# Kernel optimization log

Hardware: AMD Instinct MI355X
Metric: run time of the kernel (lower is better)

## Reference

```python
import jax, jax.numpy as jnp
import numpy as np

D = 768      # num_hiddens (hardcoded by dense1/dense2/ln in the source)
H = 12       # num_heads
NEG = -1000000.0
EPS = 1e-5


def setup_inputs() -> dict:
    key = jax.random.key(0)
    ks = jax.random.split(key, 14)
    B, Lq, Lk = 8, 1024, 1024
    s = 0.02
    return {
        "queries": jax.random.normal(ks[0], (B, Lq, D), dtype=jnp.float32),
        "keys":    jax.random.normal(ks[1], (B, Lk, D), dtype=jnp.float32),
        "values":  jax.random.normal(ks[2], (B, Lk, D), dtype=jnp.float32),
        # binary padding masks; count_nonzero along axis 1 gives valid lens
        "mask_1": jax.random.randint(ks[3], (B, Lk), 0, 2, dtype=jnp.int32),
        "mask_2": jax.random.randint(ks[4], (B, Lq), 0, 2, dtype=jnp.int32),
        # projection weights stored as [in, out] (torch Linear is y = x @ W.T)
        "Wq": jax.random.normal(ks[5], (D, D), dtype=jnp.float32) * s,
        "Wk": jax.random.normal(ks[6], (D, D), dtype=jnp.float32) * s,
        "Wv": jax.random.normal(ks[7], (D, D), dtype=jnp.float32) * s,
        "Wo": jax.random.normal(ks[8], (D, D), dtype=jnp.float32) * s,
        "d1_w": jax.random.normal(ks[9], (D, D), dtype=jnp.float32) * s,
        "d1_b": jnp.zeros((D,), dtype=jnp.float32),
        "d2_w": jax.random.normal(ks[10], (D, D), dtype=jnp.float32) * s,
        "d2_b": jnp.zeros((D,), dtype=jnp.float32),
        "ln_g": jnp.ones((D,), dtype=jnp.float32),
        "ln_b": jnp.zeros((D,), dtype=jnp.float32),
    }


def _cross_att(queries, keys, values, mask_1, mask_2,
               Wq, Wk, Wv, Wo, d1_w, d1_b, d2_w, d2_b, ln_g, ln_b):
    B, Lq, _ = queries.shape
    Lk = keys.shape[1]
    hd = D // H
    # project + split heads: [B, H, L, hd]
    q = (queries @ Wq).reshape(B, Lq, H, hd).transpose(0, 2, 1, 3)
    k = (keys    @ Wk).reshape(B, Lk, H, hd).transpose(0, 2, 1, 3)
    v = (values  @ Wv).reshape(B, Lk, H, hd).transpose(0, 2, 1, 3)
    scores = jnp.einsum('bhqd,bhkd->bhqk', q, k) / jnp.sqrt(jnp.float32(hd))
    # dual-axis prefix mask from nonzero counts
    vl1 = jnp.sum(mask_1 != 0, axis=1)  # [B], masks key axis
    vl2 = jnp.sum(mask_2 != 0, axis=1)  # [B], masks query axis
    col_ok = jnp.arange(Lk)[None, None, None, :] < vl1[:, None, None, None]
    row_ok = jnp.arange(Lq)[None, None, :, None] < vl2[:, None, None, None]
    scores = jnp.where(col_ok & row_ok, scores, NEG)
    attn = jax.nn.softmax(scores, axis=-1)
    out = jnp.einsum('bhqk,bhkd->bhqd', attn, v)
    out = out.transpose(0, 2, 1, 3).reshape(B, Lq, D)
    mha = out @ Wo
    ffn = jax.nn.relu(mha @ d1_w + d1_b) @ d2_w + d2_b
    x = ffn + mha  # dropout is identity in eval
    mu = jnp.mean(x, axis=-1, keepdims=True)
    var = jnp.mean(jnp.square(x - mu), axis=-1, keepdims=True)
    return (x - mu) / jnp.sqrt(var + EPS) * ln_g + ln_b


def reference(queries, keys, values, mask_1, mask_2,
              Wq, Wk, Wv, Wo, d1_w, d1_b, d2_w, d2_b, ln_g, ln_b):
    return _cross_att(queries, keys, values, mask_1, mask_2,
                      Wq, Wk, Wv, Wo, d1_w, d1_b, d2_w, d2_b, ln_g, ln_b)
```

## Files before the change

### kernel.cpp

```cpp
#include <hip/hip_runtime.h>
#include <hip/hip_bf16.h>
#include <type_traits>

#define DM   768
#define NH   12
#define HD   64
#define BATCH 8
#define SEQ  1024
#define NROWS (BATCH * SEQ)

typedef short bf16x8 __attribute__((ext_vector_type(8)));
typedef float f32x4 __attribute__((ext_vector_type(4)));

__device__ inline unsigned short f2b(float x) {
    union { float f; unsigned int u; } v; v.f = x;
    return (unsigned short)((v.u + 0x8000u) >> 16);
}
__device__ inline unsigned int f2b2(float lo, float hi) {
    union { float f; unsigned int u; } a, b; a.f = lo; b.f = hi;
    return __builtin_amdgcn_perm(b.u + 0x8000u, a.u + 0x8000u, 0x07060302u);
}
__device__ inline float b2f(unsigned short u) {
    union { float f; unsigned int x; } v; v.x = ((unsigned int)u) << 16;
    return v.f;
}

__device__ inline void gld16(const unsigned short* g, unsigned short* l) {
    __builtin_amdgcn_global_load_lds(
        (const __attribute__((address_space(1))) unsigned int*)g,
        (__attribute__((address_space(3))) unsigned int*)l, 16, 0, 0);
}

__global__ __launch_bounds__(256) void prep_kernel(const float* __restrict__ w0,
                                                   const float* __restrict__ w1,
                                                   const float* __restrict__ w2,
                                                   const float* __restrict__ w3,
                                                   const float* __restrict__ w4,
                                                   const float* __restrict__ w5,
                                                   unsigned short* __restrict__ wt,
                                                   const int* __restrict__ m1,
                                                   const int* __restrict__ m2,
                                                   int* __restrict__ lens) {
    const int z = blockIdx.z;
    const int t = threadIdx.x;

    if (z < 6) {
        __shared__ float tile[32][33];
        const float* W = (z == 0) ? w0 : (z == 1) ? w1 : (z == 2) ? w2
                       : (z == 3) ? w3 : (z == 4) ? w4 : w5;
        unsigned short* Wt = wt + (size_t)z * DM * DM;
        const int n0 = blockIdx.x * 32;
        const int k0 = blockIdx.y * 32;
        const int tx = t & 31;
        const int ty = t >> 5;
#pragma unroll
        for (int r = 0; r < 4; ++r)
            tile[ty + 8 * r][tx] = W[(size_t)(k0 + ty + 8 * r) * DM + n0 + tx];
        __syncthreads();
#pragma unroll
        for (int r = 0; r < 4; ++r)
            Wt[(size_t)(n0 + ty + 8 * r) * DM + k0 + tx] = f2b(tile[tx][ty + 8 * r]);
        return;
    }

    if (blockIdx.y == 12) {
        if (blockIdx.x >= 16) return;
        __shared__ int redi[256];
        const int bid = blockIdx.x;
        const int b = bid & 7;
        const int* m = (bid < 8) ? m1 : m2;
        int cnt = 0;
        for (int i = t; i < SEQ; i += 256) cnt += (m[b * SEQ + i] != 0) ? 1 : 0;
        redi[t] = cnt;
        __syncthreads();
        for (int off = 128; off > 0; off >>= 1) {
            if (t < off) redi[t] += redi[t + off];
            __syncthreads();
        }
        if (t == 0) lens[bid] = redi[0];
        return;
    }

    if (blockIdx.x >= 12 || blockIdx.y >= 12) return;
    {
        __shared__ __align__(16) unsigned short As[64][40];
        __shared__ __align__(16) unsigned short Bs[64][40];
        unsigned short* out = wt + (size_t)6 * DM * DM;
        const float* Wo = w3;
        const float* d1w = w4;
        const int mb = blockIdx.x * 64;
        const int nb = blockIdx.y * 64;
        const int wid = t >> 6, lane = t & 63;
        const int quad = lane >> 4, l16 = lane & 15;
        const int bk = t >> 3, bn = (t & 7) * 8;
        const int am = t >> 2, ak = (t & 3) * 8;

        f32x4 acc[4];
#pragma unroll
        for (int c = 0; c < 4; ++c) acc[c] = (f32x4){0.f, 0.f, 0.f, 0.f};

        for (int j0 = 0; j0 < DM; j0 += 32) {
            {
                const float* s = &d1w[(size_t)(j0 + bk) * DM + mb + bn];
                float4 f0 = ((const float4*)s)[0];
                float4 f1 = ((const float4*)s)[1];
                As[bn + 0][bk] = f2b(f0.x); As[bn + 1][bk] = f2b(f0.y);
                As[bn + 2][bk] = f2b(f0.z); As[bn + 3][bk] = f2b(f0.w);
                As[bn + 4][bk] = f2b(f1.x); As[bn + 5][bk] = f2b(f1.y);
                As[bn + 6][bk] = f2b(f1.z); As[bn + 7][bk] = f2b(f1.w);
            }
            {
                const float* s = &Wo[(size_t)(nb + am) * DM + j0 + ak];
                float4 f0 = ((const float4*)s)[0];
                float4 f1 = ((const float4*)s)[1];
                uint4 p;
                p.x = f2b2(f0.x, f0.y); p.y = f2b2(f0.z, f0.w);
                p.z = f2b2(f1.x, f1.y); p.w = f2b2(f1.z, f1.w);
                *(uint4*)&Bs[am][ak] = p;
            }
            __syncthreads();
            bf16x8 av = *(const bf16x8*)&As[16 * wid + l16][quad * 8];
#pragma unroll
            for (int c = 0; c < 4; ++c) {
                bf16x8 bv = *(const bf16x8*)&Bs[16 * c + l16][quad * 8];
                acc[c] = __builtin_amdgcn_mfma_f32_16x16x32_bf16(av, bv, acc[c], 0, 0, 0);
            }
            __syncthreads();
        }
#pragma unroll
        for (int c = 0; c < 4; ++c) {
            const int col = nb + 16 * c + l16;
#pragma unroll
            for (int r = 0; r < 4; ++r) {
                const int row = mb + 16 * wid + quad * 4 + r;
                out[(size_t)row * DM + col] = f2b(acc[c][r]);
            }
        }
    }
}

__global__ __launch_bounds__(256) void cvt_in(const float* __restrict__ q,
                                              const float* __restrict__ k,
                                              const float* __restrict__ v,
                                              unsigned short* __restrict__ oq,
                                              unsigned short* __restrict__ ok,
                                              unsigned short* __restrict__ ov) {
    const int g = blockIdx.y;
    const float* src = (g == 0) ? q : (g == 1) ? k : v;
    unsigned short* dst = (g == 0) ? oq : (g == 1) ? ok : ov;
    const size_t i = ((size_t)blockIdx.x * 256 + threadIdx.x) * 8;
    float4 f0 = ((const float4*)(src + i))[0];
    float4 f1 = ((const float4*)(src + i))[1];
    uint4 p;
    p.x = f2b2(f0.x, f0.y); p.y = f2b2(f0.z, f0.w);
    p.z = f2b2(f1.x, f1.y); p.w = f2b2(f1.z, f1.w);
    *(uint4*)(dst + i) = p;
}

__global__ __launch_bounds__(256) void qkv_gemm(const unsigned short* __restrict__ aq,
                                                const unsigned short* __restrict__ akk,
                                                const unsigned short* __restrict__ av_,
                                                const unsigned short* __restrict__ wt,
                                                unsigned short* __restrict__ c0,
                                                unsigned short* __restrict__ c1,
                                                unsigned short* __restrict__ c2) {
    __shared__ __align__(16) unsigned short As[128][32];
    __shared__ __align__(16) unsigned short Ws[128][32];

    const int t = threadIdx.x;
    const int g = blockIdx.y / 6;
    const int m0 = blockIdx.x * 128;
    const int n0 = (blockIdx.y % 6) * 128;
    const unsigned short* A = (g == 0) ? aq : (g == 1) ? akk : av_;
    const unsigned short* Wt = wt + (size_t)g * DM * DM;
    unsigned short* C = (g == 0) ? c0 : (g == 1) ? c1 : c2;

    const int w = t >> 6, lane = t & 63;
    const int quad = lane >> 4, l16 = lane & 15;
    const int wm = w & 1, wn = w >> 1;
    const int srow = 16 * w + (lane >> 2);
    const int scol = 8 * (lane & 3);

    f32x4 acc[4][4];
#pragma unroll
    for (int i = 0; i < 4; ++i)
#pragma unroll
        for (int j = 0; j < 4; ++j) acc[i][j] = (f32x4){0.f, 0.f, 0.f, 0.f};

    for (int k0 = 0; k0 < DM; k0 += 32) {
#pragma unroll
        for (int j = 0; j < 2; ++j) {
            gld16(&A[(size_t)(m0 + srow + 64 * j) * DM + k0 + scol],
                  &As[16 * w + 64 * j][0]);
            gld16(&Wt[(size_t)(n0 + srow + 64 * j) * DM + k0 + scol],
                  &Ws[16 * w + 64 * j][0]);
        }
        __syncthreads();

        bf16x8 av[4], bv[4];
#pragma unroll
        for (int i = 0; i < 4; ++i)
            av[i] = *(const bf16x8*)&As[wm * 64 + 16 * i + l16][quad * 8];
#pragma unroll
        for (int i = 0; i < 4; ++i)
            bv[i] = *(const bf16x8*)&Ws[wn * 64 + 16 * i + l16][quad * 8];
#pragma unroll
        for (int i = 0; i < 4; ++i)
#pragma unroll
            for (int j = 0; j < 4; ++j)
                acc[i][j] = __builtin_amdgcn_mfma_f32_16x16x32_bf16(av[i], bv[j], acc[i][j], 0, 0, 0);
        __syncthreads();
    }

#pragma unroll
    for (int i = 0; i < 4; ++i)
#pragma unroll
        for (int j = 0; j < 4; ++j) {
            const int gn = n0 + wn * 64 + 16 * j + l16;
#pragma unroll
            for (int r = 0; r < 4; ++r) {
                const int gm = m0 + wm * 64 + 16 * i + quad * 4 + r;
                C[(size_t)gm * DM + gn] = f2b(acc[i][j][r]);
            }
        }
}

template <typename CT>
__global__ __launch_bounds__(256) void gemm_bf(const unsigned short* __restrict__ A,
                                               const unsigned short* __restrict__ Wt,
                                               CT* __restrict__ C,
                                               const float* __restrict__ bias,
                                               const unsigned short* __restrict__ res,
                                               int relu) {
    __shared__ __align__(16) unsigned short As[128][32];
    __shared__ __align__(16) unsigned short Ws[128][32];

    const int t = threadIdx.x;
    const int m0 = blockIdx.x * 128;
    const int n0 = blockIdx.y * 128;
    const int w = t >> 6, lane = t & 63;
    const int quad = lane >> 4, l16 = lane & 15;
    const int wm = w & 1, wn = w >> 1;
    const int srow = 16 * w + (lane >> 2);
    const int scol = 8 * (lane & 3);

    f32x4 acc[4][4];
#pragma unroll
    for (int i = 0; i < 4; ++i)
#pragma unroll
        for (int j = 0; j < 4; ++j) acc[i][j] = (f32x4){0.f, 0.f, 0.f, 0.f};

    for (int k0 = 0; k0 < DM; k0 += 32) {
#pragma unroll
        for (int j = 0; j < 2; ++j) {
            gld16(&A[(size_t)(m0 + srow + 64 * j) * DM + k0 + scol],
                  &As[16 * w + 64 * j][0]);
            gld16(&Wt[(size_t)(n0 + srow + 64 * j) * DM + k0 + scol],
                  &Ws[16 * w + 64 * j][0]);
        }
        __syncthreads();

        bf16x8 av[4], bv[4];
#pragma unroll
        for (int i = 0; i < 4; ++i)
            av[i] = *(const bf16x8*)&As[wm * 64 + 16 * i + l16][quad * 8];
#pragma unroll
        for (int i = 0; i < 4; ++i)
            bv[i] = *(const bf16x8*)&Ws[wn * 64 + 16 * i + l16][quad * 8];
#pragma unroll
        for (int i = 0; i < 4; ++i)
#pragma unroll
            for (int j = 0; j < 4; ++j)
                acc[i][j] = __builtin_amdgcn_mfma_f32_16x16x32_bf16(av[i], bv[j], acc[i][j], 0, 0, 0);
        __syncthreads();
    }

#pragma unroll
    for (int i = 0; i < 4; ++i)
#pragma unroll
        for (int j = 0; j < 4; ++j) {
            const int gn = n0 + wn * 64 + 16 * j + l16;
            const float badd = bias ? bias[gn] : 0.0f;
#pragma unroll
            for (int r = 0; r < 4; ++r) {
                const int gm = m0 + wm * 64 + 16 * i + quad * 4 + r;
                float cv = acc[i][j][r] + badd;
                if (relu) cv = fmaxf(cv, 0.0f);
                if (res) cv += b2f(res[(size_t)gm * DM + gn]);
                if constexpr (std::is_same<CT, float>::value) {
                    C[(size_t)gm * DM + gn] = cv;
                } else {
                    C[(size_t)gm * DM + gn] = f2b(cv);
                }
            }
        }
}

__global__ __launch_bounds__(256) void gemm_mh(const unsigned short* __restrict__ A,
                                               const unsigned short* __restrict__ wt,
                                               unsigned short* __restrict__ cm,
                                               unsigned short* __restrict__ ch,
                                               const float* __restrict__ d1b) {
    __shared__ __align__(16) unsigned short As[128][32];
    __shared__ __align__(16) unsigned short Ws[128][32];

    const int t = threadIdx.x;
    const int unit = blockIdx.y / 6;
    const unsigned short* Wt = wt + (size_t)(unit ? 6 : 3) * DM * DM;
    unsigned short* C = unit ? ch : cm;
    const int m0 = blockIdx.x * 128;
    const int n0 = (blockIdx.y % 6) * 128;
    const int w = t >> 6, lane = t & 63;
    const int quad = lane >> 4, l16 = lane & 15;
    const int wm = w & 1, wn = w >> 1;
    const int srow = 16 * w + (lane >> 2);
    const int scol = 8 * (lane & 3);

    f32x4 acc[4][4];
#pragma unroll
    for (int i = 0; i < 4; ++i)
#pragma unroll
        for (int j = 0; j < 4; ++j) acc[i][j] = (f32x4){0.f, 0.f, 0.f, 0.f};

    for (int k0 = 0; k0 < DM; k0 += 32) {
#pragma unroll
        for (int j = 0; j < 2; ++j) {
            gld16(&A[(size_t)(m0 + srow + 64 * j) * DM + k0 + scol],
                  &As[16 * w + 64 * j][0]);
            gld16(&Wt[(size_t)(n0 + srow + 64 * j) * DM + k0 + scol],
                  &Ws[16 * w + 64 * j][0]);
        }
        __syncthreads();

        bf16x8 av[4], bv[4];
#pragma unroll
        for (int i = 0; i < 4; ++i)
            av[i] = *(const bf16x8*)&As[wm * 64 + 16 * i + l16][quad * 8];
#pragma unroll
        for (int i = 0; i < 4; ++i)
            bv[i] = *(const bf16x8*)&Ws[wn * 64 + 16 * i + l16][quad * 8];
#pragma unroll
        for (int i = 0; i < 4; ++i)
#pragma unroll
            for (int j = 0; j < 4; ++j)
                acc[i][j] = __builtin_amdgcn_mfma_f32_16x16x32_bf16(av[i], bv[j], acc[i][j], 0, 0, 0);
        __syncthreads();
    }

#pragma unroll
    for (int i = 0; i < 4; ++i)
#pragma unroll
        for (int j = 0; j < 4; ++j) {
            const int gn = n0 + wn * 64 + 16 * j + l16;
            const float badd = unit ? d1b[gn] : 0.0f;
#pragma unroll
            for (int r = 0; r < 4; ++r) {
                const int gm = m0 + wm * 64 + 16 * i + quad * 4 + r;
                float cv = acc[i][j][r] + badd;
                if (unit) cv = fmaxf(cv, 0.0f);
                C[(size_t)gm * DM + gn] = f2b(cv);
            }
        }
}

__global__ __launch_bounds__(256) void attn_mfma(const unsigned short* Q,
                                                 const unsigned short* __restrict__ K,
                                                 const unsigned short* __restrict__ V,
                                                 unsigned short* O,
                                                 const int* __restrict__ lens) {
    __shared__ __align__(16) unsigned short Ks[64][72];
    __shared__ __align__(16) unsigned short Vt[64][72];
    __shared__ __align__(16) unsigned short Ps[4][16][72];

    const int t = threadIdx.x;
    const int bid = blockIdx.x;
    const int q0 = (bid & 15) * 64;
    const int h = (bid >> 4) % NH;
    const int b = bid / (16 * NH);
    const int vl1 = lens[b];
    const int vl2 = lens[8 + b];
    const int wid = t >> 6;
    const int lane = t & 63;
    const int quad = lane >> 4;
    const int l16 = lane & 15;

    bf16x8 qa0, qa1;
    {
        const unsigned short* qp =
            &Q[(size_t)(b * SEQ + q0 + 16 * wid + l16) * DM + h * HD + quad * 8];
        qa0 = *(const bf16x8*)qp;
        qa1 = *(const bf16x8*)(qp + 32);
    }

    f32x4 o[4];
#pragma unroll
    for (int ct = 0; ct < 4; ++ct) o[ct] = (f32x4){0.f, 0.f, 0.f, 0.f};
    float suml[4];
    bool rbad[4];
#pragma unroll
    for (int r = 0; r < 4; ++r) {
        suml[r] = 0.0f;
        rbad[r] = ((q0 + 16 * wid + quad * 4 + r) >= vl2) || (vl1 == 0);
    }

    const int kkr = t >> 3;
    const int khc = (t & 7) * 8;
    const unsigned short* kbase = &K[(size_t)(b * SEQ) * DM + h * HD];
    const unsigned short* vbase = &V[(size_t)(b * SEQ) * DM + h * HD];

    uint4 kr0 = *(const uint4*)&kbase[(size_t)kkr * DM + khc];
    uint4 kr1 = *(const uint4*)&kbase[(size_t)(kkr + 32) * DM + khc];
    uint4 vr0 = *(const uint4*)&vbase[(size_t)lane * DM + wid * 16];
    uint4 vr1 = *(const uint4*)&vbase[(size_t)lane * DM + wid * 16 + 8];

    const int k2 = l16 >> 2;

    for (int tile = 0; tile < 16; ++tile) {
        const int c0 = tile * 64;
        *(uint4*)&Ks[kkr][khc] = kr0;
        *(uint4*)&Ks[kkr + 32][khc] = kr1;
        {
            union { uint4 u; unsigned short s[8]; } va, vb;
            va.u = vr0; vb.u = vr1;
#pragma unroll
            for (int j = 0; j < 8; ++j) Vt[wid * 16 + j][lane] = va.s[j];
#pragma unroll
            for (int j = 0; j < 8; ++j) Vt[wid * 16 + 8 + j][lane] = vb.s[j];
        }
        __syncthreads();

        if (tile < 15) {
            const int c1 = c0 + 64;
            kr0 = *(const uint4*)&kbase[(size_t)(c1 + kkr) * DM + khc];
            kr1 = *(const uint4*)&kbase[(size_t)(c1 + kkr + 32) * DM + khc];
            vr0 = *(const uint4*)&vbase[(size_t)(c1 + lane) * DM + wid * 16];
            vr1 = *(const uint4*)&vbase[(size_t)(c1 + lane) * DM + wid * 16 + 8];
        }

        f32x4 s[4];
#pragma unroll
        for (int ct = 0; ct < 4; ++ct) {
            f32x4 acc = (f32x4){0.f, 0.f, 0.f, 0.f};
            bf16x8 b0v = *(const bf16x8*)&Ks[16 * ct + l16][quad * 8];
            bf16x8 b1v = *(const bf16x8*)&Ks[16 * ct + l16][32 + quad * 8];
            acc = __builtin_amdgcn_mfma_f32_16x16x32_bf16(qa0, b0v, acc, 0, 0, 0);
            acc = __builtin_amdgcn_mfma_f32_16x16x32_bf16(qa1, b1v, acc, 0, 0, 0);
            s[ct] = acc;
        }
#pragma unroll
        for (int ct = 0; ct < 4; ++ct) {
            const bool kok = (c0 + 16 * ct + l16) < vl1;
#pragma unroll
            for (int r = 0; r < 4; ++r) {
                float e = __expf(s[ct][r] * 0.125f);
                float p = kok ? e : 0.0f;
                p = rbad[r] ? 1.0f : p;
                s[ct][r] = p;
                suml[r] += p;
            }
        }
#pragma unroll
        for (int ct = 0; ct < 4; ++ct) {
            const int gidx = 2 * ct + (l16 >> 3);
            const int c = l16 & 7;
            const int gs = (gidx ^ quad) * 8 + c;
#pragma unroll
            for (int r = 0; r < 4; ++r)
                Ps[wid][quad * 4 + r][gs] = f2b(s[ct][r]);
        }
        bf16x8 pa0 = *(const bf16x8*)&Ps[wid][l16][(quad ^ k2) * 8];
        bf16x8 pa1 = *(const bf16x8*)&Ps[wid][l16][((4 + quad) ^ k2) * 8];
#pragma unroll
        for (int ct = 0; ct < 4; ++ct) {
            bf16x8 vb0 = *(const bf16x8*)&Vt[16 * ct + l16][quad * 8];
            bf16x8 vb1 = *(const bf16x8*)&Vt[16 * ct + l16][32 + quad * 8];
            o[ct] = __builtin_amdgcn_mfma_f32_16x16x32_bf16(pa0, vb0, o[ct], 0, 0, 0);
            o[ct] = __builtin_amdgcn_mfma_f32_16x16x32_bf16(pa1, vb1, o[ct], 0, 0, 0);
        }
        __syncthreads();
    }

#pragma unroll
    for (int d = 1; d < 16; d <<= 1) {
#pragma unroll
        for (int r = 0; r < 4; ++r) suml[r] += __shfl_xor(suml[r], d, 64);
    }
#pragma unroll
    for (int r = 0; r < 4; ++r) {
        float inv = 1.0f / suml[r];
        const size_t row = (size_t)(b * SEQ + q0 + 16 * wid + quad * 4 + r);
#pragma unroll
        for (int ct = 0; ct < 4; ++ct) {
            O[row * DM + h * HD + 16 * ct + l16] = f2b(o[ct][r] * inv);
        }
    }
}

__global__ __launch_bounds__(256) void ln_kernel(float* __restrict__ X,
                                                 const float* __restrict__ g,
                                                 const float* __restrict__ bvec) {
    __shared__ float red[256];
    const int row = blockIdx.x;
    const int t = threadIdx.x;
    float* xr = X + (size_t)row * DM;
    float x0 = xr[t];
    float x1 = xr[t + 256];
    float x2 = xr[t + 512];
    red[t] = x0 + x1 + x2;
    __syncthreads();
    for (int off = 128; off > 0; off >>= 1) {
        if (t < off) red[t] += red[t + off];
        __syncthreads();
    }
    float mu = red[0] * (1.0f / 768.0f);
    __syncthreads();
    float d0 = x0 - mu, d1 = x1 - mu, d2 = x2 - mu;
    red[t] = d0 * d0 + d1 * d1 + d2 * d2;
    __syncthreads();
    for (int off = 128; off > 0; off >>= 1) {
        if (t < off) red[t] += red[t + off];
        __syncthreads();
    }
    float rstd = rsqrtf(red[0] * (1.0f / 768.0f) + 1e-5f);
    xr[t]       = d0 * rstd * g[t]       + bvec[t];
    xr[t + 256] = d1 * rstd * g[t + 256] + bvec[t + 256];
    xr[t + 512] = d2 * rstd * g[t + 512] + bvec[t + 512];
}

extern "C" void kernel_launch(void* const* d_in, const int* in_sizes, int n_in,
                              void* d_out, int out_size, void* d_ws, size_t ws_size,
                              hipStream_t stream) {
    const float* queries = (const float*)d_in[0];
    const float* keys    = (const float*)d_in[1];
    const float* values  = (const float*)d_in[2];
    const int* mask1 = (const int*)d_in[3];
    const int* mask2 = (const int*)d_in[4];
    const float* Wq  = (const float*)d_in[5];
    const float* Wk  = (const float*)d_in[6];
    const float* Wv  = (const float*)d_in[7];
    const float* Wo  = (const float*)d_in[8];
    const float* d1w = (const float*)d_in[9];
    const float* d1b = (const float*)d_in[10];
    const float* d2w = (const float*)d_in[11];
    const float* d2b = (const float*)d_in[12];
    const float* lng = (const float*)d_in[13];
    const float* lnb = (const float*)d_in[14];

    char* ws = (char*)d_ws;
    int* lens = (int*)ws;
    const size_t NB = (size_t)NROWS * DM * sizeof(unsigned short);
    const size_t WT = (size_t)DM * DM;
    unsigned short* b0 = (unsigned short*)(ws + 256);
    unsigned short* b1 = (unsigned short*)(ws + 256 + NB);
    unsigned short* b2 = (unsigned short*)(ws + 256 + 2 * NB);
    unsigned short* wt = (unsigned short*)(ws + 256 + 3 * NB);
    unsigned short* aq = (unsigned short*)(ws + 256 + 3 * NB + 7 * WT * sizeof(unsigned short));
    unsigned short* ak = aq + NROWS * (size_t)DM;
    unsigned short* av = ak + NROWS * (size_t)DM;
    float* xout = (float*)d_out;

    prep_kernel<<<dim3(24, 24, 7), 256, 0, stream>>>(Wq, Wk, Wv, Wo, d1w, d2w,
                                                     wt, mask1, mask2, lens);
    cvt_in<<<dim3(NROWS * DM / 8 / 256, 3), 256, 0, stream>>>(queries, keys, values,
                                                              aq, ak, av);

    qkv_gemm<<<dim3(64, 18), 256, 0, stream>>>(aq, ak, av, wt, b0, b1, b2);

    attn_mfma<<<16 * NH * BATCH, 256, 0, stream>>>(b0, b1, b2, b0, lens);

    gemm_mh<<<dim3(64, 12), 256, 0, stream>>>(b0, wt, b1, b2, d1b);

    gemm_bf<float><<<dim3(64, 6), 256, 0, stream>>>(b2, wt + 5 * WT, xout, d2b, b1, 0);

    ln_kernel<<<NROWS, 256, 0, stream>>>(xout, lng, lnb);
}
```

Baseline: 346.2 us.

## Pre-transpose V and double-buffer K/V tiles with async LDS loads in attention

```diff
diff --git a/kernel.cpp b/kernel.cpp
--- a/kernel.cpp
+++ b/kernel.cpp
@@ -157,6 +157,33 @@
     *(uint4*)(dst + i) = p;
 }
 
+__global__ __launch_bounds__(256) void vtr_kernel(const unsigned short* __restrict__ vin,
+                                                  unsigned short* __restrict__ vt) {
+    __shared__ unsigned short T[64][72];
+    const int t = threadIdx.x;
+    const int s0 = blockIdx.x * 64;
+    const int bh = blockIdx.y;
+    const int b = bh / NH, h = bh % NH;
+    {
+        const int i = t >> 2, c = t & 3;
+        const unsigned short* src = vin + (size_t)(b * SEQ + s0 + i) * DM + h * HD + c * 16;
+        uint4 a0 = ((const uint4*)src)[0];
+        uint4 a1 = ((const uint4*)src)[1];
+        *(uint4*)&T[i][c * 16] = a0;
+        *(uint4*)&T[i][c * 16 + 8] = a1;
+    }
+    __syncthreads();
+    {
+        const int d = t & 63, c = t >> 6;
+        union { uint4 u[2]; unsigned short s[16]; } pk;
+#pragma unroll
+        for (int j = 0; j < 16; ++j) pk.s[j] = T[c * 16 + j][d];
+        unsigned short* dst = vt + (size_t)(bh * HD + d) * SEQ + s0 + c * 16;
+        ((uint4*)dst)[0] = pk.u[0];
+        ((uint4*)dst)[1] = pk.u[1];
+    }
+}
+
 __global__ __launch_bounds__(256) void qkv_gemm(const unsigned short* __restrict__ aq,
                                                 const unsigned short* __restrict__ akk,
                                                 const unsigned short* __restrict__ av_,
@@ -174,6 +201,7 @@
     const unsigned short* A = (g == 0) ? aq : (g == 1) ? akk : av_;
     const unsigned short* Wt = wt + (size_t)g * DM * DM;
     unsigned short* C = (g == 0) ? c0 : (g == 1) ? c1 : c2;
+    const float cs = (g == 0) ? 0.18033688f : 1.0f;
 
     const int w = t >> 6, lane = t & 63;
     const int quad = lane >> 4, l16 = lane & 15;
@@ -220,7 +248,7 @@
 #pragma unroll
             for (int r = 0; r < 4; ++r) {
                 const int gm = m0 + wm * 64 + 16 * i + quad * 4 + r;
-                C[(size_t)gm * DM + gn] = f2b(acc[i][j][r]);
+                C[(size_t)gm * DM + gn] = f2b(acc[i][j][r] * cs);
             }
         }
 }
@@ -365,11 +393,11 @@
 
 __global__ __launch_bounds__(256) void attn_mfma(const unsigned short* Q,
                                                  const unsigned short* __restrict__ K,
-                                                 const unsigned short* __restrict__ V,
+                                                 const unsigned short* __restrict__ Vt,
                                                  unsigned short* O,
                                                  const int* __restrict__ lens) {
-    __shared__ __align__(16) unsigned short Ks[64][72];
-    __shared__ __align__(16) unsigned short Vt[64][72];
+    __shared__ __align__(16) unsigned short Ks[2][64][64];
+    __shared__ __align__(16) unsigned short Vs[2][64][64];
     __shared__ __align__(16) unsigned short Ps[4][16][72];
 
     const int t = threadIdx.x;
@@ -403,46 +431,42 @@
         rbad[r] = ((q0 + 16 * wid + quad * 4 + r) >= vl2) || (vl1 == 0);
     }
 
-    const int kkr = t >> 3;
-    const int khc = (t & 7) * 8;
-    const unsigned short* kbase = &K[(size_t)(b * SEQ) * DM + h * HD];
-    const unsigned short* vbase = &V[(size_t)(b * SEQ) * DM + h * HD];
-
-    uint4 kr0 = *(const uint4*)&kbase[(size_t)kkr * DM + khc];
-    uint4 kr1 = *(const uint4*)&kbase[(size_t)(kkr + 32) * DM + khc];
-    uint4 vr0 = *(const uint4*)&vbase[(size_t)lane * DM + wid * 16];
-    uint4 vr1 = *(const uint4*)&vbase[(size_t)lane * DM + wid * 16 + 8];
+    const int ri = lane >> 3;
+    const int gsw = ((lane & 7) ^ ri) * 8;
+    const unsigned short* kb = K + (size_t)(b * SEQ) * DM + h * HD + gsw;
+    const unsigned short* vb = Vt + ((size_t)(b * NH + h) * HD) * SEQ + gsw;
+
+#pragma unroll
+    for (int j = 0; j < 2; ++j) {
+        const int rr = 16 * wid + 8 * j + ri;
+        gld16(&kb[(size_t)rr * DM], &Ks[0][16 * wid + 8 * j][0]);
+        gld16(&vb[(size_t)rr * SEQ], &Vs[0][16 * wid + 8 * j][0]);
+    }
 
     const int k2 = l16 >> 2;
+    const int sw0 = (quad ^ (l16 & 7)) * 8;
+    const int sw1 = ((4 + quad) ^ (l16 & 7)) * 8;
 
     for (int tile = 0; tile < 16; ++tile) {
+        const int buf = tile & 1;
         const int c0 = tile * 64;
-        *(uint4*)&Ks[kkr][khc] = kr0;
-        *(uint4*)&Ks[kkr + 32][khc] = kr1;
-        {
-            union { uint4 u; unsigned short s[8]; } va, vb;
-            va.u = vr0; vb.u = vr1;
-#pragma unroll
-            for (int j = 0; j < 8; ++j) Vt[wid * 16 + j][lane] = va.s[j];
-#pragma unroll
-            for (int j = 0; j < 8; ++j) Vt[wid * 16 + 8 + j][lane] = vb.s[j];
-        }
         __syncthreads();
 
         if (tile < 15) {
-            const int c1 = c0 + 64;
-            kr0 = *(const uint4*)&kbase[(size_t)(c1 + kkr) * DM + khc];
-            kr1 = *(const uint4*)&kbase[(size_t)(c1 + kkr + 32) * DM + khc];
-            vr0 = *(const uint4*)&vbase[(size_t)(c1 + lane) * DM + wid * 16];
-            vr1 = *(const uint4*)&vbase[(size_t)(c1 + lane) * DM + wid * 16 + 8];
+#pragma unroll
+            for (int j = 0; j < 2; ++j) {
+                const int rr = 16 * wid + 8 * j + ri;
+                gld16(&kb[(size_t)(c0 + 64 + rr) * DM], &Ks[buf ^ 1][16 * wid + 8 * j][0]);
+                gld16(&vb[(size_t)rr * SEQ + c0 + 64], &Vs[buf ^ 1][16 * wid + 8 * j][0]);
+            }
         }
 
         f32x4 s[4];
 #pragma unroll
         for (int ct = 0; ct < 4; ++ct) {
             f32x4 acc = (f32x4){0.f, 0.f, 0.f, 0.f};
-            bf16x8 b0v = *(const bf16x8*)&Ks[16 * ct + l16][quad * 8];
-            bf16x8 b1v = *(const bf16x8*)&Ks[16 * ct + l16][32 + quad * 8];
+            bf16x8 b0v = *(const bf16x8*)&Ks[buf][16 * ct + l16][sw0];
+            bf16x8 b1v = *(const bf16x8*)&Ks[buf][16 * ct + l16][sw1];
             acc = __builtin_amdgcn_mfma_f32_16x16x32_bf16(qa0, b0v, acc, 0, 0, 0);
             acc = __builtin_amdgcn_mfma_f32_16x16x32_bf16(qa1, b1v, acc, 0, 0, 0);
             s[ct] = acc;
@@ -452,7 +476,7 @@
             const bool kok = (c0 + 16 * ct + l16) < vl1;
 #pragma unroll
             for (int r = 0; r < 4; ++r) {
-                float e = __expf(s[ct][r] * 0.125f);
+                float e = exp2f(s[ct][r]);
                 float p = kok ? e : 0.0f;
                 p = rbad[r] ? 1.0f : p;
                 s[ct][r] = p;
@@ -472,12 +496,11 @@
         bf16x8 pa1 = *(const bf16x8*)&Ps[wid][l16][((4 + quad) ^ k2) * 8];
 #pragma unroll
         for (int ct = 0; ct < 4; ++ct) {
-            bf16x8 vb0 = *(const bf16x8*)&Vt[16 * ct + l16][quad * 8];
-            bf16x8 vb1 = *(const bf16x8*)&Vt[16 * ct + l16][32 + quad * 8];
+            bf16x8 vb0 = *(const bf16x8*)&Vs[buf][16 * ct + l16][sw0];
+            bf16x8 vb1 = *(const bf16x8*)&Vs[buf][16 * ct + l16][sw1];
             o[ct] = __builtin_amdgcn_mfma_f32_16x16x32_bf16(pa0, vb0, o[ct], 0, 0, 0);
             o[ct] = __builtin_amdgcn_mfma_f32_16x16x32_bf16(pa1, vb1, o[ct], 0, 0, 0);
         }
-        __syncthreads();
     }
 
 #pragma unroll
@@ -555,8 +578,9 @@
     unsigned short* b2 = (unsigned short*)(ws + 256 + 2 * NB);
     unsigned short* wt = (unsigned short*)(ws + 256 + 3 * NB);
     unsigned short* aq = (unsigned short*)(ws + 256 + 3 * NB + 7 * WT * sizeof(unsigned short));
-    unsigned short* ak = aq + NROWS * (size_t)DM;
-    unsigned short* av = ak + NROWS * (size_t)DM;
+    unsigned short* ak = aq + (size_t)NROWS * DM;
+    unsigned short* av = ak + (size_t)NROWS * DM;
+    unsigned short* vtg = av + (size_t)NROWS * DM;
     float* xout = (float*)d_out;
 
     prep_kernel<<<dim3(24, 24, 7), 256, 0, stream>>>(Wq, Wk, Wv, Wo, d1w, d2w,
@@ -566,7 +590,9 @@
 
     qkv_gemm<<<dim3(64, 18), 256, 0, stream>>>(aq, ak, av, wt, b0, b1, b2);
 
-    attn_mfma<<<16 * NH * BATCH, 256, 0, stream>>>(b0, b1, b2, b0, lens);
+    vtr_kernel<<<dim3(16, 96), 256, 0, stream>>>(b2, vtg);
+
+    attn_mfma<<<16 * NH * BATCH, 256, 0, stream>>>(b0, b1, vtg, b0, lens);
 
     gemm_mh<<<dim3(64, 12), 256, 0, stream>>>(b0, wt, b1, b2, d1b);
 
```

After: 366.3 us. +5.8%, slower.
